# Kernel optimization log

Measured on AMD Instinct MI355X. Metric: run time of the kernel, lower is better.

Reference implementation:

```python
import jax, jax.numpy as jnp
import numpy as np

B, G, D, L, NH = 4, 30, 320, 4, 8
DK = D // NH
S = G * G
FF = 4 * D
EPS = 1e-5

FLOAT_KEYS = ['pe', 'in_emb_w', 'in_emb_b', 'wq', 'bq', 'wk', 'bk', 'wv', 'bv', 'wo', 'bo',
              'ln_a_g', 'ln_a_b', 'dist_emb', 'dir_emb', 'w_rot', 'b_rot', 'w_refl', 'b_refl',
              'w_tr', 'b_tr', 'w_sc', 'b_sc', 'tn_w1', 'tn_b1', 'tn_w2', 'tn_b2', 'tn_w3', 'tn_b3',
              'ff_w1', 'ff_b1', 'ff_w2', 'ff_b2', 'ln2_g', 'ln2_b', 'ck1', 'cb1', 'ck3', 'cb3',
              'ck5', 'cb5', 'ck7', 'cb7', 'fus_w', 'fus_b', 'op_w1', 'op_b1', 'op_w2', 'op_b2',
              'op_w3', 'op_b3']


def _make_pe():
    # Faithful vectorization of GeometricPositionalEncoding's triple loop.
    pe = np.zeros((G, G, D), dtype=np.float32)
    i = np.arange(0, D // 2, 2)                       # 0,2,...,158
    div = 10000.0 ** (i / D)
    h = np.arange(G, dtype=np.float64)
    sh = np.sin(h[:, None] / div)[:, None, :]
    ch = np.cos(h[:, None] / div)[:, None, :]
    pe[:, :, i] = sh
    pe[:, :, i + 1] = ch
    sw = np.sin(h[:, None] / div)[None, :, :]
    cw = np.cos(h[:, None] / div)[None, :, :]
    pe[:, :, i + D // 2] = sw
    pe[:, :, i + D // 2 + 1] = cw
    hh, ww = np.meshgrid(np.arange(G), np.arange(G), indexing='ij')
    c = G // 2
    pe[:, :, -4] = np.sqrt((hh - c) ** 2 + (ww - c) ** 2) / G   # overwrites last 4 dims, as in torch
    pe[:, :, -3] = hh / G
    pe[:, :, -2] = ww / G
    pe[:, :, -1] = (hh + ww) / (2 * G)
    return pe


def _make_geo_indices():
    # Precompute _compute_geometric_bias index tables (distance bin, direction octant).
    idx = np.arange(S)
    hc, wc = idx // G, idx % G
    dh = hc[None, :] - hc[:, None]                    # h2 - h1 at [i, j]
    dw = wc[None, :] - wc[:, None]
    dist = np.minimum(np.sqrt(dh ** 2 + dw ** 2).astype(np.int32), 59)
    ang = np.arctan2(dh.astype(np.float64), dw.astype(np.float64))
    dirn = ((ang + np.pi) / (2 * np.pi / 8)).astype(np.int32) % 8
    dirn[(dh == 0) & (dw == 0)] = 0
    return dist.astype(np.int32), dirn.astype(np.int32)


def _ln(x, g, b):
    m = x.mean(-1, keepdims=True)
    v = ((x - m) ** 2).mean(-1, keepdims=True)
    return (x - m) * jax.lax.rsqrt(v + EPS) * g + b


def _gelu(x):
    return jax.nn.gelu(x, approximate=False)  # torch nn.GELU default (erf)


def _forward(p, input_grid, dist_idx, dir_idx):
    x = jax.nn.one_hot(input_grid[:, 0], 10, dtype=jnp.float32)   # [B,G,G,10]
    x = x @ p['in_emb_w'] + p['in_emb_b']                          # [B,G,G,D]
    x = x + p['pe'][None]
    scale = 1.0 / np.sqrt(DK)
    for l in range(L):
        xs = x.reshape(B, S, D)
        def heads(w, b):
            return (xs @ w + b).reshape(B, S, NH, DK).transpose(0, 2, 1, 3)
        q = heads(p['wq'][l], p['bq'][l])
        k = heads(p['wk'][l], p['bk'][l])
        v = heads(p['wv'][l], p['bv'][l])
        # geometric bias via embedding gathers: [S,S,NH] -> [NH,S,S]
        bias = p['dist_emb'][l][dist_idx] + p['dir_emb'][l][dir_idx]
        scores = jnp.einsum('bhsd,bhtd->bhst', q, k) * scale + bias.transpose(2, 0, 1)[None]
        attn = jax.nn.softmax(scores, axis=-1)
        out = jnp.einsum('bhst,bhtd->bhsd', attn, v).transpose(0, 2, 1, 3).reshape(B, S, D)
        xs = _ln(out @ p['wo'][l] + p['bo'][l] + xs, p['ln_a_g'][l], p['ln_a_b'][l])
        # geometric transformation module
        g = xs.mean(1)                                              # [B,D] global mean over H,W
        tp = jnp.concatenate([
            jax.nn.softmax(g @ p['w_rot'][l] + p['b_rot'][l], axis=-1),
            jax.nn.softmax(g @ p['w_refl'][l] + p['b_refl'][l], axis=-1),
            jnp.tanh(g @ p['w_tr'][l] + p['b_tr'][l]),
            jax.nn.softmax(g @ p['w_sc'][l] + p['b_sc'][l], axis=-1)], axis=-1)   # [B,17]
        ti = jnp.concatenate([xs, jnp.broadcast_to(tp[:, None, :], (B, S, 17))], axis=-1)
        t = _gelu(ti @ p['tn_w1'][l] + p['tn_b1'][l])
        t = _gelu(t @ p['tn_w2'][l] + p['tn_b2'][l])
        t = t @ p['tn_w3'][l] + p['tn_b3'][l]
        xs = xs + 0.3 * t
        # feed-forward with post-LN residual
        f = _gelu(xs @ p['ff_w1'][l] + p['ff_b1'][l]) @ p['ff_w2'][l] + p['ff_b2'][l]
        xs = _ln(f + xs, p['ln2_g'][l], p['ln2_b'][l])
        x = xs.reshape(B, G, G, D)
    # multiscale conv fusion (NHWC, SAME padding == torch padding=k//2 for odd k)
    dn = ('NHWC', 'HWIO', 'NHWC')
    feats = [jax.nn.relu(jax.lax.conv_general_dilated(x, p['ck%d' % kk], (1, 1), 'SAME',
                                                      dimension_numbers=dn) + p['cb%d' % kk])
             for kk in (1, 3, 5, 7)]
    fused = jnp.concatenate(feats, axis=-1) @ p['fus_w'] + p['fus_b']
    h1 = _gelu(fused @ p['op_w1'] + p['op_b1'])
    h2 = _gelu(h1 @ p['op_w2'] + p['op_b2'])
    return h2 @ p['op_w3'] + p['op_b3']                            # [B,G,G,10] logits


def setup_inputs():
    key = jax.random.key(0)
    ks = iter(jax.random.split(key, 80))
    w = lambda *s: (0.02 * jax.random.normal(next(ks), s)).astype(jnp.float32)
    z = lambda *s: jnp.zeros(s, jnp.float32)
    inp = dict(
        input_grid=jax.random.randint(next(ks), (B, 1, G, G), 0, 10, dtype=jnp.int32),
        pe=jnp.asarray(_make_pe()),
        in_emb_w=w(10, D), in_emb_b=z(D),
        wq=w(L, D, D), bq=z(L, D), wk=w(L, D, D), bk=z(L, D),
        wv=w(L, D, D), bv=z(L, D), wo=w(L, D, D), bo=z(L, D),
        ln_a_g=jnp.ones((L, D), jnp.float32), ln_a_b=z(L, D),
        dist_emb=w(L, 60, NH), dir_emb=w(L, 8, NH),
        w_rot=w(L, D, 4), b_rot=z(L, 4), w_refl=w(L, D, 8), b_refl=z(L, 8),
        w_tr=w(L, D, 2), b_tr=z(L, 2), w_sc=w(L, D, 3), b_sc=z(L, 3),
        tn_w1=w(L, D + 17, 2 * D), tn_b1=z(L, 2 * D),
        tn_w2=w(L, 2 * D, D), tn_b2=z(L, D),
        tn_w3=w(L, D, D), tn_b3=z(L, D),
        ff_w1=w(L, D, FF), ff_b1=z(L, FF), ff_w2=w(L, FF, D), ff_b2=z(L, D),
        ln2_g=jnp.ones((L, D), jnp.float32), ln2_b=z(L, D),
        ck1=w(1, 1, D, D), cb1=z(D), ck3=w(3, 3, D, D), cb3=z(D),
        ck5=w(5, 5, D, D), cb5=z(D), ck7=w(7, 7, D, D), cb7=z(D),
        fus_w=w(4 * D, D), fus_b=z(D),
        op_w1=w(D, D // 2), op_b1=z(D // 2),
        op_w2=w(D // 2, D // 4), op_b2=z(D // 4),
        op_w3=w(D // 4, 10), op_b3=z(10),
    )
    di, dr = _make_geo_indices()
    inp['dist_idx'] = jnp.asarray(di)
    inp['dir_idx'] = jnp.asarray(dr)
    return inp


def reference(input_grid, dist_idx, dir_idx, pe, in_emb_w, in_emb_b, wq, bq, wk, bk, wv, bv, wo, bo,
              ln_a_g, ln_a_b, dist_emb, dir_emb, w_rot, b_rot, w_refl, b_refl, w_tr, b_tr, w_sc, b_sc,
              tn_w1, tn_b1, tn_w2, tn_b2, tn_w3, tn_b3, ff_w1, ff_b1, ff_w2, ff_b2, ln2_g, ln2_b,
              ck1, cb1, ck3, cb3, ck5, cb5, ck7, cb7, fus_w, fus_b,
              op_w1, op_b1, op_w2, op_b2, op_w3, op_b3):
    p = dict(zip(FLOAT_KEYS, (pe, in_emb_w, in_emb_b, wq, bq, wk, bk, wv, bv, wo, bo,
                              ln_a_g, ln_a_b, dist_emb, dir_emb, w_rot, b_rot, w_refl, b_refl,
                              w_tr, b_tr, w_sc, b_sc, tn_w1, tn_b1, tn_w2, tn_b2, tn_w3, tn_b3,
                              ff_w1, ff_b1, ff_w2, ff_b2, ln2_g, ln2_b, ck1, cb1, ck3, cb3,
                              ck5, cb5, ck7, cb7, fus_w, fus_b, op_w1, op_b1, op_w2, op_b2,
                              op_w3, op_b3)))
    return _forward(p, input_grid, dist_idx, dir_idx)
```

## Files before the change

### kernel.cpp

```cpp
#include <hip/hip_runtime.h>
#include <hip/hip_bf16.h>

#define BB 4
#define GG_ 30
#define DD 320
#define LL 4
#define NHH 8
#define DKK 40
#define SS 900
#define BS 3600
#define FFD 1280
#define LDK 72

typedef __attribute__((ext_vector_type(8))) short short8;
typedef __attribute__((ext_vector_type(4))) short short4v;
typedef __attribute__((ext_vector_type(4))) float f32x4;

__device__ __forceinline__ float gelu_f(float x) {
    return 0.5f * x * (1.0f + erff(x * 0.70710678118654752f));
}

__device__ __forceinline__ float bfbits2f(short b) {
    return __uint_as_float(((unsigned)(unsigned short)b) << 16);
}

__device__ __forceinline__ void convt_tile(const float* __restrict__ s,
                                           __hip_bfloat16* __restrict__ d,
                                           int K, int N, int Kpad, int kb, int nb) {
    __shared__ float t[32][33];
    const int tx = threadIdx.x, ty = threadIdx.y;
#pragma unroll
    for (int i = 0; i < 4; ++i) {
        int k = kb + ty + i * 8, n = nb + tx;
        t[ty + i * 8][tx] = (k < K && n < N) ? s[(size_t)k * N + n] : 0.f;
    }
    __syncthreads();
#pragma unroll
    for (int i = 0; i < 4; ++i) {
        int n = nb + ty + i * 8, k = kb + tx;
        if (n < N && k < Kpad) d[(size_t)n * Kpad + k] = __float2bfloat16(t[tx][ty + i * 8]);
    }
}

__global__ __launch_bounds__(256) void allconvt_kernel(
    const float* wo, const float* tnw1, const float* tnw2, const float* tnw3,
    const float* ffw1, const float* ffw2, const float* ck1, const float* ck3,
    const float* ck5, const float* ck7, const float* fusw, const float* opw1,
    __hip_bfloat16* WOT, __hip_bfloat16* TN1T, __hip_bfloat16* TN2T, __hip_bfloat16* TN3T,
    __hip_bfloat16* FF1T, __hip_bfloat16* FF2T, __hip_bfloat16* CK1T, __hip_bfloat16* CK3T,
    __hip_bfloat16* CK5T, __hip_bfloat16* CK7T, __hip_bfloat16* FUST, __hip_bfloat16* OP1T) {
    const int bid = blockIdx.x;
    const float* s; __hip_bfloat16* d;
    int K, N, Kpad, gx, per, local, sS, dS;
    if (bid < 400)        { local = bid;         s = wo;   d = WOT;  K = 320;  N = 320;  Kpad = 320;  sS = 102400; dS = 102400; gx = 10;  per = 100; }
    else if (bid < 1360)  { local = bid - 400;   s = tnw1; d = TN1T; K = 337;  N = 640;  Kpad = 384;  sS = 215680; dS = 245760; gx = 12;  per = 240; }
    else if (bid < 2160)  { local = bid - 1360;  s = tnw2; d = TN2T; K = 640;  N = 320;  Kpad = 640;  sS = 204800; dS = 204800; gx = 20;  per = 200; }
    else if (bid < 2560)  { local = bid - 2160;  s = tnw3; d = TN3T; K = 320;  N = 320;  Kpad = 320;  sS = 102400; dS = 102400; gx = 10;  per = 100; }
    else if (bid < 4160)  { local = bid - 2560;  s = ffw1; d = FF1T; K = 320;  N = 1280; Kpad = 320;  sS = 409600; dS = 409600; gx = 10;  per = 400; }
    else if (bid < 5760)  { local = bid - 4160;  s = ffw2; d = FF2T; K = 1280; N = 320;  Kpad = 1280; sS = 409600; dS = 409600; gx = 40;  per = 400; }
    else if (bid < 5860)  { local = bid - 5760;  s = ck1;  d = CK1T; K = 320;  N = 320;  Kpad = 320;  sS = 0; dS = 0; gx = 10;  per = 100; }
    else if (bid < 6760)  { local = bid - 5860;  s = ck3;  d = CK3T; K = 2880; N = 320;  Kpad = 2880; sS = 0; dS = 0; gx = 90;  per = 900; }
    else if (bid < 9260)  { local = bid - 6760;  s = ck5;  d = CK5T; K = 8000; N = 320;  Kpad = 8000; sS = 0; dS = 0; gx = 250; per = 2500; }
    else if (bid < 14160) { local = bid - 9260;  s = ck7;  d = CK7T; K = 15680; N = 320; Kpad = 15680; sS = 0; dS = 0; gx = 490; per = 4900; }
    else if (bid < 14560) { local = bid - 14160; s = fusw; d = FUST; K = 1280; N = 320;  Kpad = 1280; sS = 0; dS = 0; gx = 40;  per = 400; }
    else                  { local = bid - 14560; s = opw1; d = OP1T; K = 320;  N = 160;  Kpad = 320;  sS = 0; dS = 0; gx = 10;  per = 50; }
    const int mat = local / per, rem = local - mat * per;
    const int kb = (rem % gx) * 32, nb = (rem / gx) * 32;
    convt_tile(s + (size_t)mat * sS, d + (size_t)mat * dS, K, N, Kpad, kb, nb);
}

__global__ __launch_bounds__(256) void qkvconvt_kernel(const float* __restrict__ wq,
                                                       const float* __restrict__ wk,
                                                       const float* __restrict__ wv,
                                                       __hip_bfloat16* __restrict__ dst) {
    __shared__ float t[32][33];
    const int z = blockIdx.z, l = z / 3, wsel = z % 3;
    const float* s = (wsel == 0 ? wq : wsel == 1 ? wk : wv) + (size_t)l * 102400;
    __hip_bfloat16* d = dst + (size_t)l * 307200 + wsel * 102400;
    const int kb = blockIdx.x * 32, nb = blockIdx.y * 32;
    const int tx = threadIdx.x, ty = threadIdx.y;
#pragma unroll
    for (int i = 0; i < 4; ++i) {
        int k = kb + ty + i * 8, n = nb + tx;
        t[ty + i * 8][tx] = s[(size_t)k * 320 + n];
    }
    __syncthreads();
#pragma unroll
    for (int i = 0; i < 4; ++i) {
        int n = nb + ty + i * 8, k = kb + tx;
        d[(size_t)n * 320 + k] = __float2bfloat16(t[tx][ty + i * 8]);
    }
}

__global__ void embed_kernel(const int* __restrict__ grid, const float* __restrict__ pe,
                             const float* __restrict__ ew, const float* __restrict__ eb,
                             float* __restrict__ x, __hip_bfloat16* __restrict__ xb) {
    int idx = blockIdx.x * 256 + threadIdx.x;
    int m = idx / DD, d = idx % DD;
    int gv = grid[m];
    float v = ew[gv * DD + d] + eb[d] + pe[(m % SS) * DD + d];
    x[idx] = v;
    xb[idx] = __float2bfloat16(v);
}

__global__ __launch_bounds__(256) void mgemm_kernel(
    const __hip_bfloat16* __restrict__ A, int lda,
    const __hip_bfloat16* __restrict__ Wt, int ldw,
    const float* __restrict__ bias, const float* __restrict__ biasB, const float* __restrict__ biasC,
    const float* __restrict__ res, int ldr,
    float alpha, float* __restrict__ Cf, float* __restrict__ Cf2,
    __hip_bfloat16* __restrict__ Cb, int ldc,
    int M, int N, int K, int act) {
    __shared__ short As[128 * LDK];
    __shared__ short Bs[64 * LDK];
    const int tid = threadIdx.x;
    const int m0 = blockIdx.y * 128, n0 = blockIdx.x * 64;
    const int kb0 = blockIdx.z * K;
    float* __restrict__ CfO = (blockIdx.z == 0) ? Cf : Cf2;
    const int lane = tid & 63;
    const int w = tid >> 6, wm = w >> 1, wn = w & 1;
    const int rbase = tid >> 3, q8 = (tid & 7) * 8;
    f32x4 acc[4][2];
    const f32x4 fz = {0.f, 0.f, 0.f, 0.f};
#pragma unroll
    for (int mi = 0; mi < 4; ++mi)
#pragma unroll
        for (int ni = 0; ni < 2; ++ni) acc[mi][ni] = fz;
    const short8 zz = {0, 0, 0, 0, 0, 0, 0, 0};
    for (int k0 = 0; k0 < K; k0 += 64) {
#pragma unroll
        for (int c = 0; c < 4; ++c) {
            int r = c * 32 + rbase, m = m0 + r;
            short8 v = zz;
            if (m < M) v = *(const short8*)((const short*)A + (size_t)m * lda + kb0 + k0 + q8);
            *(short8*)(As + r * LDK + q8) = v;
        }
#pragma unroll
        for (int c = 0; c < 2; ++c) {
            int r = c * 32 + rbase, n = n0 + r;
            short8 v = zz;
            if (n < N) v = *(const short8*)((const short*)Wt + (size_t)n * ldw + kb0 + k0 + q8);
            *(short8*)(Bs + r * LDK + q8) = v;
        }
        __syncthreads();
#pragma unroll
        for (int ks = 0; ks < 64; ks += 32) {
            const int kb = ks + (lane >> 4) * 8;
            short8 af[4], bf[2];
#pragma unroll
            for (int mi = 0; mi < 4; ++mi)
                af[mi] = *(const short8*)(As + (wm * 64 + mi * 16 + (lane & 15)) * LDK + kb);
#pragma unroll
            for (int ni = 0; ni < 2; ++ni)
                bf[ni] = *(const short8*)(Bs + (wn * 32 + ni * 16 + (lane & 15)) * LDK + kb);
#pragma unroll
            for (int mi = 0; mi < 4; ++mi)
#pragma unroll
                for (int ni = 0; ni < 2; ++ni)
                    acc[mi][ni] = __builtin_amdgcn_mfma_f32_16x16x32_bf16(af[mi], bf[ni], acc[mi][ni], 0, 0, 0);
        }
        __syncthreads();
    }
    const int col0 = n0 + wn * 32 + (lane & 15);
    const int rloc = (lane >> 4) * 4;
#pragma unroll
    for (int mi = 0; mi < 4; ++mi) {
#pragma unroll
        for (int ni = 0; ni < 2; ++ni) {
            int col = col0 + ni * 16;
            if (col >= N) continue;
            float bv;
            if (biasC) bv = (col < 320) ? bias[col] : (col < 640) ? biasB[col - 320] : biasC[col - 640];
            else bv = bias ? bias[col] : 0.f;
#pragma unroll
            for (int r = 0; r < 4; ++r) {
                int row = m0 + wm * 64 + mi * 16 + rloc + r;
                if (row >= M) continue;
                float v = acc[mi][ni][r] + bv;
                if (act == 1) v = gelu_f(v);
                else if (act == 2) v = fmaxf(v, 0.f);
                v *= alpha;
                if (res) v += res[(size_t)row * ldr + col];
                if (CfO) CfO[(size_t)row * ldc + col] = v;
                if (Cb) Cb[(size_t)row * ldc + col] = __float2bfloat16(v);
            }
        }
    }
}

template <int KS>
__global__ __launch_bounds__(256) void mconv_kernel(
    const __hip_bfloat16* __restrict__ P, const __hip_bfloat16* __restrict__ Wt,
    __hip_bfloat16* __restrict__ part, int kh0step) {
    const int K = KS * KS * DD;
    const int OFF = 3 - KS / 2;
    const int kh0 = blockIdx.z * kh0step;
    const int nkh = (KS - kh0 < kh0step) ? (KS - kh0) : kh0step;
    const int Ksub = nkh * KS * DD;
    const int wbase = kh0 * KS * DD;
    __hip_bfloat16* __restrict__ Cp = part + (size_t)blockIdx.z * BS * DD;
    __shared__ short As[128 * LDK];
    __shared__ short Bs[64 * LDK];
    const int tid = threadIdx.x;
    const int m0 = blockIdx.y * 128, n0 = blockIdx.x * 64;
    const int lane = tid & 63;
    const int w = tid >> 6, wm = w >> 1, wn = w & 1;
    const int rbase = tid >> 3, q8 = (tid & 7) * 8;
    f32x4 acc[4][2];
    const f32x4 fz = {0.f, 0.f, 0.f, 0.f};
#pragma unroll
    for (int mi = 0; mi < 4; ++mi)
#pragma unroll
        for (int ni = 0; ni < 2; ++ni) acc[mi][ni] = fz;
    const short8 zz = {0, 0, 0, 0, 0, 0, 0, 0};
    for (int k0 = 0; k0 < Ksub; k0 += 64) {
#pragma unroll
        for (int c = 0; c < 4; ++c) {
            int r = c * 32 + rbase, m = m0 + r;
            int k = k0 + q8;
            int ci = k % DD, t = k / DD;
            int kw = t % KS, kh = kh0 + t / KS;
            short8 v = zz;
            if (m < BS) {
                int b = m / SS, hw = m % SS, oh = hw / GG_, ow = hw % GG_;
                int ih = oh + kh + OFF, iw = ow + kw + OFF;
                v = *(const short8*)((const short*)P + (((b * 36 + ih) * 36 + iw) * DD + ci));
            }
            *(short8*)(As + r * LDK + q8) = v;
        }
#pragma unroll
        for (int c = 0; c < 2; ++c) {
            int r = c * 32 + rbase, n = n0 + r;
            short8 v = *(const short8*)((const short*)Wt + (size_t)n * K + wbase + k0 + q8);
            *(short8*)(Bs + r * LDK + q8) = v;
        }
        __syncthreads();
#pragma unroll
        for (int ks = 0; ks < 64; ks += 32) {
            const int kb = ks + (lane >> 4) * 8;
            short8 af[4], bf[2];
#pragma unroll
            for (int mi = 0; mi < 4; ++mi)
                af[mi] = *(const short8*)(As + (wm * 64 + mi * 16 + (lane & 15)) * LDK + kb);
#pragma unroll
            for (int ni = 0; ni < 2; ++ni)
                bf[ni] = *(const short8*)(Bs + (wn * 32 + ni * 16 + (lane & 15)) * LDK + kb);
#pragma unroll
            for (int mi = 0; mi < 4; ++mi)
#pragma unroll
                for (int ni = 0; ni < 2; ++ni)
                    acc[mi][ni] = __builtin_amdgcn_mfma_f32_16x16x32_bf16(af[mi], bf[ni], acc[mi][ni], 0, 0, 0);
        }
        __syncthreads();
    }
    const int col0 = n0 + wn * 32 + (lane & 15);
    const int rloc = (lane >> 4) * 4;
#pragma unroll
    for (int mi = 0; mi < 4; ++mi) {
#pragma unroll
        for (int ni = 0; ni < 2; ++ni) {
            int col = col0 + ni * 16;
#pragma unroll
            for (int r = 0; r < 4; ++r) {
                int row = m0 + wm * 64 + mi * 16 + rloc + r;
                if (row < BS) Cp[(size_t)row * DD + col] = __float2bfloat16(acc[mi][ni][r]);
            }
        }
    }
}

__global__ __launch_bounds__(256) void creduce_kernel(const __hip_bfloat16* __restrict__ part,
                                                      int nsplit, const float* __restrict__ bias,
                                                      __hip_bfloat16* __restrict__ outb, int ldc) {
    int idx = blockIdx.x * 256 + threadIdx.x;
    if (idx >= BS * DD / 8) return;
    int row = idx / (DD / 8), c8 = (idx % (DD / 8)) * 8;
    float s[8] = {};
    for (int p = 0; p < nsplit; ++p) {
        short8 v = *(const short8*)((const short*)part + (size_t)p * BS * DD + (size_t)row * DD + c8);
#pragma unroll
        for (int j = 0; j < 8; ++j) s[j] += bfbits2f(v[j]);
    }
    __hip_bfloat16* o = outb + (size_t)row * ldc + c8;
#pragma unroll
    for (int j = 0; j < 8; ++j) o[j] = __float2bfloat16(fmaxf(s[j] + bias[c8 + j], 0.f));
}

__global__ void pad_kernel(const __hip_bfloat16* __restrict__ xb, __hip_bfloat16* __restrict__ p) {
    int idx = blockIdx.x * 256 + threadIdx.x;
    if (idx >= BB * 36 * 36 * DD) return;
    int c = idx % DD, t = idx / DD;
    int wp = t % 36, t2 = t / 36, hp = t2 % 36, b = t2 / 36;
    __hip_bfloat16 v = __float2bfloat16(0.f);
    if (hp >= 3 && hp < 33 && wp >= 3 && wp < 33)
        v = xb[((b * SS + (hp - 3) * GG_ + (wp - 3))) * DD + c];
    p[idx] = v;
}

__global__ __launch_bounds__(256) void gemm_kernel(
    const float* __restrict__ A, int lda, const float* __restrict__ W,
    const float* __restrict__ bias, float* __restrict__ C, int ldc,
    int M, int N, int K, int act) {
    __shared__ float As[16][65];
    __shared__ float Ws[16][65];
    const int tid = threadIdx.x;
    const int m0 = blockIdx.y * 64, n0 = blockIdx.x * 64;
    const int tx = tid & 15, ty = tid >> 4;
    float acc[4][4] = {};
    const int kkA = tid & 15, mloc0 = tid >> 4;
    const int nloc = tid & 63, kk0 = tid >> 6;
    for (int k0 = 0; k0 < K; k0 += 16) {
        const int kA = k0 + kkA;
#pragma unroll
        for (int i = 0; i < 4; ++i) {
            int mloc = mloc0 + i * 16, m = m0 + mloc;
            As[kkA][mloc] = (m < M && kA < K) ? A[m * lda + kA] : 0.f;
        }
#pragma unroll
        for (int i = 0; i < 4; ++i) {
            int kk = kk0 + i * 4, k = k0 + kk, n = n0 + nloc;
            Ws[kk][nloc] = (k < K && n < N) ? W[k * N + n] : 0.f;
        }
        __syncthreads();
#pragma unroll
        for (int kk = 0; kk < 16; ++kk) {
            float a[4], b[4];
#pragma unroll
            for (int i = 0; i < 4; ++i) a[i] = As[kk][ty * 4 + i];
#pragma unroll
            for (int j = 0; j < 4; ++j) b[j] = Ws[kk][tx * 4 + j];
#pragma unroll
            for (int i = 0; i < 4; ++i)
#pragma unroll
                for (int j = 0; j < 4; ++j) acc[i][j] = fmaf(a[i], b[j], acc[i][j]);
        }
        __syncthreads();
    }
#pragma unroll
    for (int i = 0; i < 4; ++i) {
        int m = m0 + ty * 4 + i;
        if (m >= M) continue;
#pragma unroll
        for (int j = 0; j < 4; ++j) {
            int n = n0 + tx * 4 + j;
            if (n >= N) continue;
            float v = acc[i][j] + bias[n];
            if (act == 1) v = gelu_f(v);
            C[m * ldc + n] = v;
        }
    }
}

__global__ __launch_bounds__(256) void attprep_kernel(const float* __restrict__ de,
                                                      const float* __restrict__ dre,
                                                      const int* __restrict__ dist,
                                                      const int* __restrict__ dirn,
                                                      const __hip_bfloat16* __restrict__ QKV,
                                                      __hip_bfloat16* __restrict__ biasOut,
                                                      __hip_bfloat16* __restrict__ VT) {
    const int gid = blockIdx.x;
    const int tid = threadIdx.x;
    if (gid < 27000) {
        const int h = gid / 3375;
        int idx = (gid % 3375) * 256 + tid;
        int sq = idx / 960, t = idx - sq * 960;
        float v = 0.f;
        if (t < SS) v = de[dist[sq * SS + t] * NHH + h] + dre[dirn[sq * SS + t] * NHH + h];
        biasOut[((size_t)h * SS + sq) * 960 + t] = __float2bfloat16(v);
    } else {
        int idx = (gid - 27000) * 256 + tid;
        int t = idx % 960;
        int d = (idx / 960) % 48;
        int h = (idx / (960 * 48)) % NHH;
        int b = idx / (960 * 48 * NHH);
        __hip_bfloat16 v = __float2bfloat16(0.f);
        if (t < SS && d < DKK) v = QKV[((size_t)b * SS + t) * 960 + 640 + h * DKK + d];
        VT[idx] = v;
    }
}

#define LQ 56
#define LK 56
#define LV 72
#define LP 72
__global__ __launch_bounds__(256) void mattn_kernel(
    const __hip_bfloat16* __restrict__ Qg, const __hip_bfloat16* __restrict__ Kg,
    const __hip_bfloat16* __restrict__ VTg, const __hip_bfloat16* __restrict__ BIASg,
    __hip_bfloat16* __restrict__ AO) {
    const int qt = blockIdx.x, h = blockIdx.y, b = blockIdx.z;
    const int tid = threadIdx.x, lane = tid & 63, w = tid >> 6;
    const int lhi = lane >> 4, llo = lane & 15;
    __shared__ short Qs[64 * LQ];
    __shared__ short Ks[64 * LK];
    __shared__ short Vs[48 * LV];
    __shared__ short Ps[4][16 * LP];
    short* Ps_w = Ps[w];
    const int q0 = qt * 64;
    const short4v z4 = {0, 0, 0, 0};
    const f32x4 fz = {0.f, 0.f, 0.f, 0.f};
    const float scale = 0.15811388300841898f;

    for (int task = tid; task < 64 * 14; task += 256) {
        int r = task / 14, d0 = (task - r * 14) * 4;
        int q = q0 + r;
        short4v v = z4;
        if (q < SS && d0 < DKK)
            v = *(const short4v*)((const short*)Qg + ((size_t)b * SS + q) * 960 + h * DKK + d0);
        *(short4v*)(Qs + r * LQ + d0) = v;
    }
    __syncthreads();
    short8 qa[2];
#pragma unroll
    for (int ks = 0; ks < 2; ++ks)
        qa[ks] = *(const short8*)(Qs + (w * 16 + llo) * LQ + ks * 32 + lhi * 8);

    float mrow[4] = {-1e30f, -1e30f, -1e30f, -1e30f};
    float lrow[4] = {0.f, 0.f, 0.f, 0.f};
    f32x4 o[3] = {fz, fz, fz};
    const int qrow = q0 + w * 16 + lhi * 4;

    for (int t = 0; t < 15; ++t) {
        const int kv0 = t * 64;
        for (int task = tid; task < 64 * 14; task += 256) {
            int r = task / 14, d0 = (task - r * 14) * 4;
            int kv = kv0 + r;
            short4v v = z4;
            if (kv < SS && d0 < DKK)
                v = *(const short4v*)((const short*)Kg + ((size_t)b * SS + kv) * 960 + h * DKK + d0);
            *(short4v*)(Ks + r * LK + d0) = v;
        }
        for (int task = tid; task < 48 * 16; task += 256) {
            int r = task / 16, c4 = (task - r * 16) * 4;
            short4v v = *(const short4v*)((const short*)VTg +
                         (((size_t)b * NHH + h) * 48 + r) * 960 + kv0 + c4);
            *(short4v*)(Vs + r * LV + c4) = v;
        }
        __syncthreads();
        f32x4 s[4] = {fz, fz, fz, fz};
#pragma unroll
        for (int ks = 0; ks < 2; ++ks) {
#pragma unroll
            for (int ni = 0; ni < 4; ++ni) {
                short8 kb = *(const short8*)(Ks + (ni * 16 + llo) * LK + ks * 32 + lhi * 8);
                s[ni] = __builtin_amdgcn_mfma_f32_16x16x32_bf16(qa[ks], kb, s[ni], 0, 0, 0);
            }
        }
#pragma unroll
        for (int ni = 0; ni < 4; ++ni) {
            int col = kv0 + ni * 16 + llo;
#pragma unroll
            for (int r = 0; r < 4; ++r) {
                int qc = qrow + r; if (qc > SS - 1) qc = SS - 1;
                float v = s[ni][r] * scale +
                          __bfloat162float(BIASg[((size_t)h * SS + qc) * 960 + col]);
                s[ni][r] = (col < SS) ? v : -1e30f;
            }
        }
        float rmax[4], psum[4], corr[4];
#pragma unroll
        for (int r = 0; r < 4; ++r)
            rmax[r] = fmaxf(fmaxf(s[0][r], s[1][r]), fmaxf(s[2][r], s[3][r]));
#pragma unroll
        for (int off = 1; off < 16; off <<= 1)
#pragma unroll
            for (int r = 0; r < 4; ++r)
                rmax[r] = fmaxf(rmax[r], __shfl_xor(rmax[r], off));
#pragma unroll
        for (int r = 0; r < 4; ++r) {
            float mnew = fmaxf(mrow[r], rmax[r]);
            corr[r] = expf(mrow[r] - mnew);
            mrow[r] = mnew;
            float ps = 0.f;
#pragma unroll
            for (int ni = 0; ni < 4; ++ni) {
                float p = expf(s[ni][r] - mnew);
                s[ni][r] = p;
                ps += p;
            }
            psum[r] = ps;
        }
#pragma unroll
        for (int off = 1; off < 16; off <<= 1)
#pragma unroll
            for (int r = 0; r < 4; ++r) psum[r] += __shfl_xor(psum[r], off);
#pragma unroll
        for (int r = 0; r < 4; ++r) lrow[r] = lrow[r] * corr[r] + psum[r];
#pragma unroll
        for (int nj = 0; nj < 3; ++nj)
#pragma unroll
            for (int r = 0; r < 4; ++r) o[nj][r] *= corr[r];
#pragma unroll
        for (int ni = 0; ni < 4; ++ni)
#pragma unroll
            for (int r = 0; r < 4; ++r)
                ((__hip_bfloat16*)Ps_w)[(lhi * 4 + r) * LP + ni * 16 + llo] =
                    __float2bfloat16(s[ni][r]);
#pragma unroll
        for (int ks = 0; ks < 2; ++ks) {
            short8 pa = *(const short8*)(Ps_w + llo * LP + ks * 32 + lhi * 8);
#pragma unroll
            for (int nj = 0; nj < 3; ++nj) {
                short8 vb = *(const short8*)(Vs + (nj * 16 + llo) * LV + ks * 32 + lhi * 8);
                o[nj] = __builtin_amdgcn_mfma_f32_16x16x32_bf16(pa, vb, o[nj], 0, 0, 0);
            }
        }
        __syncthreads();
    }
#pragma unroll
    for (int nj = 0; nj < 3; ++nj) {
        int d = nj * 16 + llo;
        if (d >= DKK) continue;
#pragma unroll
        for (int r = 0; r < 4; ++r) {
            int q = qrow + r;
            if (q < SS)
                AO[((size_t)b * SS + q) * DD + h * DKK + d] = __float2bfloat16(o[nj][r] / lrow[r]);
        }
    }
}

__global__ __launch_bounds__(320) void ln_kernel(const float* __restrict__ a,
                                                 const float* __restrict__ a2,
                                                 const float* __restrict__ cb,
                                                 const float* __restrict__ add,
                                                 const float* __restrict__ g,
                                                 const float* __restrict__ bta,
                                                 float* __restrict__ out,
                                                 __hip_bfloat16* __restrict__ outb) {
    const int row = blockIdx.x, i = threadIdx.x;
    __shared__ float red[320];
    __shared__ float s_m, s_v;
    float v = a[row * DD + i];
    if (a2) v += a2[row * DD + i];
    if (cb) v += cb[i];
    if (add) v += add[row * DD + i];
    red[i] = v;
    __syncthreads();
    if (i < 64) red[i] += red[i + 256];
    __syncthreads();
    for (int s = 128; s > 0; s >>= 1) {
        if (i < s) red[i] += red[i + s];
        __syncthreads();
    }
    if (i == 0) s_m = red[0] * (1.0f / DD);
    __syncthreads();
    const float d = v - s_m;
    red[i] = d * d;
    __syncthreads();
    if (i < 64) red[i] += red[i + 256];
    __syncthreads();
    for (int s = 128; s > 0; s >>= 1) {
        if (i < s) red[i] += red[i + s];
        __syncthreads();
    }
    if (i == 0) s_v = red[0] * (1.0f / DD);
    __syncthreads();
    float o = d * rsqrtf(s_v + 1e-5f) * g[i] + bta[i];
    out[row * DD + i] = o;
    outb[row * DD + i] = __float2bfloat16(o);
}

__global__ __launch_bounds__(256) void mpart_kernel(const float* __restrict__ xs,
                                                    float* __restrict__ mp) {
    const int b = blockIdx.y, z = blockIdx.z;
    const int d = blockIdx.x * 64 + (threadIdx.x & 63);
    const int rg = threadIdx.x >> 6;
    float s = 0.f;
    const int t0 = z * 150;
    for (int t = t0 + rg; t < t0 + 150; t += 4) s += xs[((size_t)b * SS + t) * DD + d];
    __shared__ float red[256];
    red[threadIdx.x] = s;
    __syncthreads();
    if (threadIdx.x < 128) red[threadIdx.x] += red[threadIdx.x + 128];
    __syncthreads();
    if (threadIdx.x < 64) mp[((size_t)b * 6 + z) * DD + d] = red[threadIdx.x] + red[threadIdx.x + 64];
}

__global__ __launch_bounds__(64) void tp_kernel(const float* __restrict__ mp,
                                                const float* __restrict__ wrot, const float* __restrict__ brot,
                                                const float* __restrict__ wrefl, const float* __restrict__ brefl,
                                                const float* __restrict__ wtr, const float* __restrict__ btr,
                                                const float* __restrict__ wsc, const float* __restrict__ bsc,
                                                float* __restrict__ tp) {
    const int b = blockIdx.x, tid = threadIdx.x;
    __shared__ float gs[DD];
    __shared__ float raw[17];
    for (int j = tid; j < DD; j += 64) {
        float s6 = 0.f;
#pragma unroll
        for (int z = 0; z < 6; ++z) s6 += mp[((size_t)b * 6 + z) * DD + j];
        gs[j] = s6 * (1.0f / SS);
    }
    __syncthreads();
    if (tid < 17) {
        float s;
        if (tid < 4) {
            s = brot[tid];
            for (int d = 0; d < DD; ++d) s = fmaf(gs[d], wrot[d * 4 + tid], s);
        } else if (tid < 12) {
            int j = tid - 4;
            s = brefl[j];
            for (int d = 0; d < DD; ++d) s = fmaf(gs[d], wrefl[d * 8 + j], s);
        } else if (tid < 14) {
            int j = tid - 12;
            s = btr[j];
            for (int d = 0; d < DD; ++d) s = fmaf(gs[d], wtr[d * 2 + j], s);
        } else {
            int j = tid - 14;
            s = bsc[j];
            for (int d = 0; d < DD; ++d) s = fmaf(gs[d], wsc[d * 3 + j], s);
        }
        raw[tid] = s;
    }
    __syncthreads();
    if (tid == 0) {
        float mx = -1e30f;
        for (int j = 0; j < 4; ++j) mx = fmaxf(mx, raw[j]);
        float sm = 0.f, e[4];
        for (int j = 0; j < 4; ++j) { e[j] = expf(raw[j] - mx); sm += e[j]; }
        for (int j = 0; j < 4; ++j) tp[b * 17 + j] = e[j] / sm;
    } else if (tid == 1) {
        float mx = -1e30f;
        for (int j = 4; j < 12; ++j) mx = fmaxf(mx, raw[j]);
        float sm = 0.f, e[8];
        for (int j = 0; j < 8; ++j) { e[j] = expf(raw[4 + j] - mx); sm += e[j]; }
        for (int j = 0; j < 8; ++j) tp[b * 17 + 4 + j] = e[j] / sm;
    } else if (tid == 2) {
        tp[b * 17 + 12] = tanhf(raw[12]);
        tp[b * 17 + 13] = tanhf(raw[13]);
    } else if (tid == 3) {
        float mx = -1e30f;
        for (int j = 14; j < 17; ++j) mx = fmaxf(mx, raw[j]);
        float sm = 0.f, e[3];
        for (int j = 0; j < 3; ++j) { e[j] = expf(raw[14 + j] - mx); sm += e[j]; }
        for (int j = 0; j < 3; ++j) tp[b * 17 + 14 + j] = e[j] / sm;
    }
}

__global__ void concat_kernel(const __hip_bfloat16* __restrict__ xb, const float* __restrict__ tp,
                              __hip_bfloat16* __restrict__ ti) {
    int idx = blockIdx.x * 256 + threadIdx.x;
    if (idx >= BS * 384) return;
    int m = idx / 384, j = idx % 384;
    __hip_bfloat16 v;
    if (j < DD) v = xb[m * DD + j];
    else if (j < 337) v = __float2bfloat16(tp[(m / SS) * 17 + (j - DD)]);
    else v = __float2bfloat16(0.f);
    ti[idx] = v;
}

static inline void launch_mgemm(hipStream_t s, const __hip_bfloat16* A, int lda,
                                const __hip_bfloat16* Wt, int ldw, const float* bias,
                                const float* biasB, const float* biasC,
                                const float* res, int ldr, float alpha, float* Cf,
                                __hip_bfloat16* Cb, int ldc, int M, int N, int K, int act) {
    dim3 g((N + 63) / 64, (M + 127) / 128);
    mgemm_kernel<<<g, 256, 0, s>>>(A, lda, Wt, ldw, bias, biasB, biasC, res, ldr, alpha,
                                   Cf, nullptr, Cb, ldc, M, N, K, act);
}

extern "C" void kernel_launch(void* const* d_in, const int* in_sizes, int n_in,
                              void* d_out, int out_size, void* d_ws, size_t ws_size,
                              hipStream_t stream) {
    (void)in_sizes; (void)n_in; (void)out_size; (void)ws_size;
    const int* in_grid = (const int*)d_in[0];
    const float* pe = (const float*)d_in[1];
    const float* iew = (const float*)d_in[2];
    const float* ieb = (const float*)d_in[3];
    const float* wq = (const float*)d_in[4], *bq = (const float*)d_in[5];
    const float* wk = (const float*)d_in[6], *bk = (const float*)d_in[7];
    const float* wv = (const float*)d_in[8], *bv = (const float*)d_in[9];
    const float* wo = (const float*)d_in[10], *bo = (const float*)d_in[11];
    const float* lnag = (const float*)d_in[12], *lnab = (const float*)d_in[13];
    const float* dist_emb = (const float*)d_in[14], *dir_emb = (const float*)d_in[15];
    const float* wrot = (const float*)d_in[16], *brot = (const float*)d_in[17];
    const float* wrefl = (const float*)d_in[18], *brefl = (const float*)d_in[19];
    const float* wtr = (const float*)d_in[20], *btr = (const float*)d_in[21];
    const float* wsc = (const float*)d_in[22], *bsc = (const float*)d_in[23];
    const float* tnw1 = (const float*)d_in[24], *tnb1 = (const float*)d_in[25];
    const float* tnw2 = (const float*)d_in[26], *tnb2 = (const float*)d_in[27];
    const float* tnw3 = (const float*)d_in[28], *tnb3 = (const float*)d_in[29];
    const float* ffw1 = (const float*)d_in[30], *ffb1 = (const float*)d_in[31];
    const float* ffw2 = (const float*)d_in[32], *ffb2 = (const float*)d_in[33];
    const float* ln2g = (const float*)d_in[34], *ln2b = (const float*)d_in[35];
    const float* ck1 = (const float*)d_in[36], *cb1 = (const float*)d_in[37];
    const float* ck3 = (const float*)d_in[38], *cb3 = (const float*)d_in[39];
    const float* ck5 = (const float*)d_in[40], *cb5 = (const float*)d_in[41];
    const float* ck7 = (const float*)d_in[42], *cb7 = (const float*)d_in[43];
    const float* fusw = (const float*)d_in[44], *fusb = (const float*)d_in[45];
    const float* opw1 = (const float*)d_in[46], *opb1 = (const float*)d_in[47];
    const float* opw2 = (const float*)d_in[48], *opb2 = (const float*)d_in[49];
    const float* opw3 = (const float*)d_in[50], *opb3 = (const float*)d_in[51];
    const int* dist_idx = (const int*)d_in[52];
    const int* dir_idx = (const int*)d_in[53];
    float* out = (float*)d_out;

    char* base = (char*)d_ws;
    typedef __hip_bfloat16 bf;
    bf* WQKVT = (bf*)(base + 0);
    bf* WOT = (bf*)(base + 2457600);
    bf* TN1T = (bf*)(base + 3276800);
    bf* TN2T = (bf*)(base + 5242880);
    bf* TN3T = (bf*)(base + 6881280);
    bf* FF1T = (bf*)(base + 7700480);
    bf* FF2T = (bf*)(base + 10977280);
    bf* CK1T = (bf*)(base + 14254080);
    bf* CK3T = (bf*)(base + 14458880);
    bf* CK5T = (bf*)(base + 16302080);
    bf* CK7T = (bf*)(base + 21422080);
    bf* FUST = (bf*)(base + 31457280);
    bf* OP1T = (bf*)(base + 32276480);
    float* XS = (float*)(base + 32378880);
    bf* XSbf = (bf*)(base + 36986880);
    bf* QKVbf = (bf*)(base + 39290880);
    bf* VT = (bf*)(base + 46202880);
    float* P1f = (float*)(base + 39290880);
    float* R2 = (float*)(base + 53114880);
    float* TP = (float*)(base + 57728000);
    bf* CPART = (bf*)(base + 39290880);
    char* BIG = base + 57728512;
    bf* AObf = (bf*)(BIG + 0);
    float* MPart = (float*)(BIG + 0);
    bf* BIAS = (bf*)(BIG + 2764800);
    bf* TIbf = (bf*)(BIG + 0);
    bf* T1bf = (bf*)(BIG + 2764800);
    bf* T2bf = (bf*)(BIG + 7372800);
    bf* F1bf = (bf*)(BIG + 0);
    bf* PADbf = (bf*)(BIG + 0);
    bf* FEATSbf = (bf*)(BIG + 3317760);
    float* H1 = (float*)(BIG + 0);
    float* H2 = (float*)(BIG + 2304000);
    bf* R2bf = XSbf;

    dim3 cb(32, 8);
    qkvconvt_kernel<<<dim3(10, 10, 12), cb, 0, stream>>>(wq, wk, wv, WQKVT);
    allconvt_kernel<<<14610, cb, 0, stream>>>(wo, tnw1, tnw2, tnw3, ffw1, ffw2,
                                              ck1, ck3, ck5, ck7, fusw, opw1,
                                              WOT, TN1T, TN2T, TN3T, FF1T, FF2T,
                                              CK1T, CK3T, CK5T, CK7T, FUST, OP1T);

    embed_kernel<<<4500, 256, 0, stream>>>(in_grid, pe, iew, ieb, XS, XSbf);

    for (int l = 0; l < LL; ++l) {
        const int wO = l * DD * DD, bO = l * DD;
        launch_mgemm(stream, XSbf, DD, WQKVT + l * 307200, 320, bq + bO, bk + bO, bv + bO,
                     nullptr, 0, 1.f, nullptr, QKVbf, 960, BS, 960, 320, 0);
        attprep_kernel<<<32760, 256, 0, stream>>>(dist_emb + l * 60 * NHH, dir_emb + l * 8 * NHH,
                                                  dist_idx, dir_idx, QKVbf, BIAS, VT);
        mattn_kernel<<<dim3(15, NHH, BB), 256, 0, stream>>>(QKVbf, QKVbf + 320, VT, BIAS, AObf);
        launch_mgemm(stream, AObf, DD, WOT + wO, DD, bo + bO, nullptr, nullptr, XS, DD, 1.f,
                     R2, nullptr, DD, BS, DD, DD, 0);
        ln_kernel<<<BS, 320, 0, stream>>>(R2, nullptr, nullptr, nullptr, lnag + bO, lnab + bO, XS, XSbf);
        mpart_kernel<<<dim3(5, BB, 6), 256, 0, stream>>>(XS, MPart);
        tp_kernel<<<BB, 64, 0, stream>>>(MPart, wrot + l * 1280, brot + l * 4,
                                         wrefl + l * 2560, brefl + l * 8,
                                         wtr + l * 640, btr + l * 2,
                                         wsc + l * 960, bsc + l * 3, TP);
        concat_kernel<<<(BS * 384 + 255) / 256, 256, 0, stream>>>(XSbf, TP, TIbf);
        launch_mgemm(stream, TIbf, 384, TN1T + l * 245760, 384, tnb1 + l * 640, nullptr, nullptr,
                     nullptr, 0, 1.f, nullptr, T1bf, 640, BS, 640, 384, 1);
        launch_mgemm(stream, T1bf, 640, TN2T + l * 204800, 640, tnb2 + bO, nullptr, nullptr,
                     nullptr, 0, 1.f, nullptr, T2bf, DD, BS, DD, 640, 1);
        launch_mgemm(stream, T2bf, DD, TN3T + wO, DD, tnb3 + bO, nullptr, nullptr, XS, DD, 0.3f,
                     XS, XSbf, DD, BS, DD, DD, 0);
        launch_mgemm(stream, XSbf, DD, FF1T + l * 409600, DD, ffb1 + l * FFD, nullptr, nullptr,
                     nullptr, 0, 1.f, nullptr, F1bf, FFD, BS, FFD, DD, 1);
        {
            dim3 g(5, 29, 2);
            mgemm_kernel<<<g, 256, 0, stream>>>(F1bf, FFD, FF2T + l * 409600, FFD,
                                                nullptr, nullptr, nullptr, nullptr, 0, 1.f,
                                                R2, P1f, nullptr, DD, BS, DD, 640, 0);
        }
        ln_kernel<<<BS, 320, 0, stream>>>(R2, P1f, ffb2 + bO, XS, ln2g + bO, ln2b + bO, XS, XSbf);
    }

    pad_kernel<<<(BB * 36 * 36 * DD + 255) / 256, 256, 0, stream>>>(XSbf, PADbf);
    launch_mgemm(stream, XSbf, DD, CK1T, DD, cb1, nullptr, nullptr, nullptr, 0, 1.f,
                 nullptr, FEATSbf + 0, 1280, BS, DD, DD, 2);
    const int RED = (BS * DD / 8 + 255) / 256;
    mconv_kernel<3><<<dim3(5, 29, 3), 256, 0, stream>>>(PADbf, CK3T, CPART, 1);
    creduce_kernel<<<RED, 256, 0, stream>>>(CPART, 3, cb3, FEATSbf + 320, 1280);
    mconv_kernel<5><<<dim3(5, 29, 5), 256, 0, stream>>>(PADbf, CK5T, CPART, 1);
    creduce_kernel<<<RED, 256, 0, stream>>>(CPART, 5, cb5, FEATSbf + 640, 1280);
    mconv_kernel<7><<<dim3(5, 29, 7), 256, 0, stream>>>(PADbf, CK7T, CPART, 1);
    creduce_kernel<<<RED, 256, 0, stream>>>(CPART, 7, cb7, FEATSbf + 960, 1280);
    launch_mgemm(stream, FEATSbf, 1280, FUST, 1280, fusb, nullptr, nullptr, nullptr, 0, 1.f,
                 nullptr, R2bf, DD, BS, DD, 1280, 0);
    launch_mgemm(stream, R2bf, DD, OP1T, DD, opb1, nullptr, nullptr, nullptr, 0, 1.f,
                 H1, nullptr, 160, BS, 160, DD, 1);
    gemm_kernel<<<dim3(2, 57), 256, 0, stream>>>(H1, 160, opw2, opb2, H2, 80, BS, 80, 160, 1);
    gemm_kernel<<<dim3(1, 57), 256, 0, stream>>>(H2, 80, opw3, opb3, out, 10, BS, 10, 80, 0);
}
```

Baseline: 1.743 ms.

## Split attention KV loop across two wave groups and swap conv grid order

The attention kernel now runs 512 threads per block. Two groups of four waves each handle alternate 64-key tiles, and their partial softmax states (max, sum, output) are merged through shared memory at the end. This is meant to double the parallelism per query tile, since the grid is only 480 blocks. It also switches to fast __expf and widens the Q/K LDS stride to 72. Separately, the mconv kernel swaps its grid x/y mapping so M tiles vary fastest, which changes L2 reuse of weights versus activations. The attention kernel uses more LDS and adds extra syncs in exchange.

```diff
diff --git a/kernel.cpp b/kernel.cpp
--- a/kernel.cpp
+++ b/kernel.cpp
@@ -202,7 +202,7 @@
     __shared__ short As[128 * LDK];
     __shared__ short Bs[64 * LDK];
     const int tid = threadIdx.x;
-    const int m0 = blockIdx.y * 128, n0 = blockIdx.x * 64;
+    const int m0 = blockIdx.x * 128, n0 = blockIdx.y * 64;
     const int lane = tid & 63;
     const int w = tid >> 6, wm = w >> 1, wn = w & 1;
     const int rbase = tid >> 3, q8 = (tid & 7) * 8;
@@ -379,29 +379,36 @@
     }
 }
 
-#define LQ 56
-#define LK 56
+#define LQ 72
+#define LK 72
 #define LV 72
 #define LP 72
-__global__ __launch_bounds__(256) void mattn_kernel(
+__global__ __launch_bounds__(512) void mattn_kernel(
     const __hip_bfloat16* __restrict__ Qg, const __hip_bfloat16* __restrict__ Kg,
     const __hip_bfloat16* __restrict__ VTg, const __hip_bfloat16* __restrict__ BIASg,
     __hip_bfloat16* __restrict__ AO) {
     const int qt = blockIdx.x, h = blockIdx.y, b = blockIdx.z;
     const int tid = threadIdx.x, lane = tid & 63, w = tid >> 6;
+    const int wq = w & 3, ws = w >> 2;
+    const int tid2 = tid & 255;
     const int lhi = lane >> 4, llo = lane & 15;
     __shared__ short Qs[64 * LQ];
-    __shared__ short Ks[64 * LK];
-    __shared__ short Vs[48 * LV];
-    __shared__ short Ps[4][16 * LP];
+    __shared__ short Ks[2][64 * LK];
+    __shared__ short Vs[2][48 * LV];
+    __shared__ short Ps[8][16 * LP];
+    __shared__ float Lm[4][16];
+    __shared__ float Ll[4][16];
+    __shared__ float Lo[4][16][DKK];
     short* Ps_w = Ps[w];
+    short* Ks_s = Ks[ws];
+    short* Vs_s = Vs[ws];
     const int q0 = qt * 64;
     const short4v z4 = {0, 0, 0, 0};
     const f32x4 fz = {0.f, 0.f, 0.f, 0.f};
     const float scale = 0.15811388300841898f;
 
-    for (int task = tid; task < 64 * 14; task += 256) {
-        int r = task / 14, d0 = (task - r * 14) * 4;
+    for (int task = tid; task < 64 * 16; task += 512) {
+        int r = task >> 4, d0 = (task & 15) * 4;
         int q = q0 + r;
         short4v v = z4;
         if (q < SS && d0 < DKK)
@@ -412,109 +419,136 @@
     short8 qa[2];
 #pragma unroll
     for (int ks = 0; ks < 2; ++ks)
-        qa[ks] = *(const short8*)(Qs + (w * 16 + llo) * LQ + ks * 32 + lhi * 8);
+        qa[ks] = *(const short8*)(Qs + (wq * 16 + llo) * LQ + ks * 32 + lhi * 8);
 
     float mrow[4] = {-1e30f, -1e30f, -1e30f, -1e30f};
     float lrow[4] = {0.f, 0.f, 0.f, 0.f};
     f32x4 o[3] = {fz, fz, fz};
-    const int qrow = q0 + w * 16 + lhi * 4;
-
-    for (int t = 0; t < 15; ++t) {
+    const int qrow = q0 + wq * 16 + lhi * 4;
+
+    for (int tt = 0; tt < 8; ++tt) {
+        const int t = tt * 2 + ws;
         const int kv0 = t * 64;
-        for (int task = tid; task < 64 * 14; task += 256) {
-            int r = task / 14, d0 = (task - r * 14) * 4;
-            int kv = kv0 + r;
-            short4v v = z4;
-            if (kv < SS && d0 < DKK)
-                v = *(const short4v*)((const short*)Kg + ((size_t)b * SS + kv) * 960 + h * DKK + d0);
-            *(short4v*)(Ks + r * LK + d0) = v;
-        }
-        for (int task = tid; task < 48 * 16; task += 256) {
-            int r = task / 16, c4 = (task - r * 16) * 4;
-            short4v v = *(const short4v*)((const short*)VTg +
-                         (((size_t)b * NHH + h) * 48 + r) * 960 + kv0 + c4);
-            *(short4v*)(Vs + r * LV + c4) = v;
-        }
-        __syncthreads();
-        f32x4 s[4] = {fz, fz, fz, fz};
-#pragma unroll
-        for (int ks = 0; ks < 2; ++ks) {
+        if (t < 15) {
+            for (int task = tid2; task < 64 * 16; task += 256) {
+                int r = task >> 4, d0 = (task & 15) * 4;
+                int kv = kv0 + r;
+                short4v v = z4;
+                if (kv < SS && d0 < DKK)
+                    v = *(const short4v*)((const short*)Kg + ((size_t)b * SS + kv) * 960 + h * DKK + d0);
+                *(short4v*)(Ks_s + r * LK + d0) = v;
+            }
+            for (int task = tid2; task < 48 * 16; task += 256) {
+                int r = task >> 4, c4 = (task & 15) * 4;
+                short4v v = *(const short4v*)((const short*)VTg +
+                             (((size_t)b * NHH + h) * 48 + r) * 960 + kv0 + c4);
+                *(short4v*)(Vs_s + r * LV + c4) = v;
+            }
+        }
+        __syncthreads();
+        if (t < 15) {
+            f32x4 s[4] = {fz, fz, fz, fz};
+#pragma unroll
+            for (int ks = 0; ks < 2; ++ks) {
+#pragma unroll
+                for (int ni = 0; ni < 4; ++ni) {
+                    short8 kb = *(const short8*)(Ks_s + (ni * 16 + llo) * LK + ks * 32 + lhi * 8);
+                    s[ni] = __builtin_amdgcn_mfma_f32_16x16x32_bf16(qa[ks], kb, s[ni], 0, 0, 0);
+                }
+            }
 #pragma unroll
             for (int ni = 0; ni < 4; ++ni) {
-                short8 kb = *(const short8*)(Ks + (ni * 16 + llo) * LK + ks * 32 + lhi * 8);
-                s[ni] = __builtin_amdgcn_mfma_f32_16x16x32_bf16(qa[ks], kb, s[ni], 0, 0, 0);
-            }
-        }
-#pragma unroll
-        for (int ni = 0; ni < 4; ++ni) {
-            int col = kv0 + ni * 16 + llo;
+                int col = kv0 + ni * 16 + llo;
+#pragma unroll
+                for (int r = 0; r < 4; ++r) {
+                    int qc = qrow + r; if (qc > SS - 1) qc = SS - 1;
+                    float v = s[ni][r] * scale +
+                              __bfloat162float(BIASg[((size_t)h * SS + qc) * 960 + col]);
+                    s[ni][r] = (col < SS) ? v : -1e30f;
+                }
+            }
+            float rmax[4], psum[4], corr[4];
+#pragma unroll
+            for (int r = 0; r < 4; ++r)
+                rmax[r] = fmaxf(fmaxf(s[0][r], s[1][r]), fmaxf(s[2][r], s[3][r]));
+#pragma unroll
+            for (int off = 1; off < 16; off <<= 1)
+#pragma unroll
+                for (int r = 0; r < 4; ++r)
+                    rmax[r] = fmaxf(rmax[r], __shfl_xor(rmax[r], off));
 #pragma unroll
             for (int r = 0; r < 4; ++r) {
-                int qc = qrow + r; if (qc > SS - 1) qc = SS - 1;
-                float v = s[ni][r] * scale +
-                          __bfloat162float(BIASg[((size_t)h * SS + qc) * 960 + col]);
-                s[ni][r] = (col < SS) ? v : -1e30f;
-            }
-        }
-        float rmax[4], psum[4], corr[4];
-#pragma unroll
-        for (int r = 0; r < 4; ++r)
-            rmax[r] = fmaxf(fmaxf(s[0][r], s[1][r]), fmaxf(s[2][r], s[3][r]));
-#pragma unroll
-        for (int off = 1; off < 16; off <<= 1)
-#pragma unroll
-            for (int r = 0; r < 4; ++r)
-                rmax[r] = fmaxf(rmax[r], __shfl_xor(rmax[r], off));
+                float mnew = fmaxf(mrow[r], rmax[r]);
+                corr[r] = __expf(mrow[r] - mnew);
+                mrow[r] = mnew;
+                float ps = 0.f;
+#pragma unroll
+                for (int ni = 0; ni < 4; ++ni) {
+                    float p = __expf(s[ni][r] - mnew);
+                    s[ni][r] = p;
+                    ps += p;
+                }
+                psum[r] = ps;
+            }
+#pragma unroll
+            for (int off = 1; off < 16; off <<= 1)
+#pragma unroll
+                for (int r = 0; r < 4; ++r) psum[r] += __shfl_xor(psum[r], off);
+#pragma unroll
+            for (int r = 0; r < 4; ++r) lrow[r] = lrow[r] * corr[r] + psum[r];
+#pragma unroll
+            for (int nj = 0; nj < 3; ++nj)
+#pragma unroll
+                for (int r = 0; r < 4; ++r) o[nj][r] *= corr[r];
+#pragma unroll
+            for (int ni = 0; ni < 4; ++ni)
+#pragma unroll
+                for (int r = 0; r < 4; ++r)
+                    ((__hip_bfloat16*)Ps_w)[(lhi * 4 + r) * LP + ni * 16 + llo] =
+                        __float2bfloat16(s[ni][r]);
+#pragma unroll
+            for (int ks = 0; ks < 2; ++ks) {
+                short8 pa = *(const short8*)(Ps_w + llo * LP + ks * 32 + lhi * 8);
+#pragma unroll
+                for (int nj = 0; nj < 3; ++nj) {
+                    short8 vb = *(const short8*)(Vs_s + (nj * 16 + llo) * LV + ks * 32 + lhi * 8);
+                    o[nj] = __builtin_amdgcn_mfma_f32_16x16x32_bf16(pa, vb, o[nj], 0, 0, 0);
+                }
+            }
+        }
+        __syncthreads();
+    }
+    if (ws == 1) {
 #pragma unroll
         for (int r = 0; r < 4; ++r) {
-            float mnew = fmaxf(mrow[r], rmax[r]);
-            corr[r] = expf(mrow[r] - mnew);
-            mrow[r] = mnew;
-            float ps = 0.f;
-#pragma unroll
-            for (int ni = 0; ni < 4; ++ni) {
-                float p = expf(s[ni][r] - mnew);
-                s[ni][r] = p;
-                ps += p;
-            }
-            psum[r] = ps;
-        }
-#pragma unroll
-        for (int off = 1; off < 16; off <<= 1)
-#pragma unroll
-            for (int r = 0; r < 4; ++r) psum[r] += __shfl_xor(psum[r], off);
-#pragma unroll
-        for (int r = 0; r < 4; ++r) lrow[r] = lrow[r] * corr[r] + psum[r];
-#pragma unroll
-        for (int nj = 0; nj < 3; ++nj)
-#pragma unroll
-            for (int r = 0; r < 4; ++r) o[nj][r] *= corr[r];
-#pragma unroll
-        for (int ni = 0; ni < 4; ++ni)
-#pragma unroll
-            for (int r = 0; r < 4; ++r)
-                ((__hip_bfloat16*)Ps_w)[(lhi * 4 + r) * LP + ni * 16 + llo] =
-                    __float2bfloat16(s[ni][r]);
-#pragma unroll
-        for (int ks = 0; ks < 2; ++ks) {
-            short8 pa = *(const short8*)(Ps_w + llo * LP + ks * 32 + lhi * 8);
+            int lr = lhi * 4 + r;
+            if (llo == 0) { Lm[wq][lr] = mrow[r]; Ll[wq][lr] = lrow[r]; }
 #pragma unroll
             for (int nj = 0; nj < 3; ++nj) {
-                short8 vb = *(const short8*)(Vs + (nj * 16 + llo) * LV + ks * 32 + lhi * 8);
-                o[nj] = __builtin_amdgcn_mfma_f32_16x16x32_bf16(pa, vb, o[nj], 0, 0, 0);
-            }
-        }
-        __syncthreads();
-    }
-#pragma unroll
-    for (int nj = 0; nj < 3; ++nj) {
-        int d = nj * 16 + llo;
-        if (d >= DKK) continue;
+                int d = nj * 16 + llo;
+                if (d < DKK) Lo[wq][lr][d] = o[nj][r];
+            }
+        }
+    }
+    __syncthreads();
+    if (ws == 0) {
 #pragma unroll
         for (int r = 0; r < 4; ++r) {
+            int lr = lhi * 4 + r;
+            float m1 = Lm[wq][lr], l1 = Ll[wq][lr];
+            float m = fmaxf(mrow[r], m1);
+            float a0 = __expf(mrow[r] - m), a1 = __expf(m1 - m);
+            float linv = 1.f / (lrow[r] * a0 + l1 * a1);
             int q = qrow + r;
-            if (q < SS)
-                AO[((size_t)b * SS + q) * DD + h * DKK + d] = __float2bfloat16(o[nj][r] / lrow[r]);
+            if (q < SS) {
+#pragma unroll
+                for (int nj = 0; nj < 3; ++nj) {
+                    int d = nj * 16 + llo;
+                    if (d < DKK)
+                        AO[((size_t)b * SS + q) * DD + h * DKK + d] =
+                            __float2bfloat16((o[nj][r] * a0 + Lo[wq][lr][d] * a1) * linv);
+                }
+            }
         }
     }
 }
@@ -747,7 +781,7 @@
                      nullptr, 0, 1.f, nullptr, QKVbf, 960, BS, 960, 320, 0);
         attprep_kernel<<<32760, 256, 0, stream>>>(dist_emb + l * 60 * NHH, dir_emb + l * 8 * NHH,
                                                   dist_idx, dir_idx, QKVbf, BIAS, VT);
-        mattn_kernel<<<dim3(15, NHH, BB), 256, 0, stream>>>(QKVbf, QKVbf + 320, VT, BIAS, AObf);
+        mattn_kernel<<<dim3(15, NHH, BB), 512, 0, stream>>>(QKVbf, QKVbf + 320, VT, BIAS, AObf);
         launch_mgemm(stream, AObf, DD, WOT + wO, DD, bo + bO, nullptr, nullptr, XS, DD, 1.f,
                      R2, nullptr, DD, BS, DD, DD, 0);
         ln_kernel<<<BS, 320, 0, stream>>>(R2, nullptr, nullptr, nullptr, lnag + bO, lnab + bO, XS, XSbf);
@@ -778,11 +812,11 @@
     launch_mgemm(stream, XSbf, DD, CK1T, DD, cb1, nullptr, nullptr, nullptr, 0, 1.f,
                  nullptr, FEATSbf + 0, 1280, BS, DD, DD, 2);
     const int RED = (BS * DD / 8 + 255) / 256;
-    mconv_kernel<3><<<dim3(5, 29, 3), 256, 0, stream>>>(PADbf, CK3T, CPART, 1);
+    mconv_kernel<3><<<dim3(29, 5, 3), 256, 0, stream>>>(PADbf, CK3T, CPART, 1);
     creduce_kernel<<<RED, 256, 0, stream>>>(CPART, 3, cb3, FEATSbf + 320, 1280);
-    mconv_kernel<5><<<dim3(5, 29, 5), 256, 0, stream>>>(PADbf, CK5T, CPART, 1);
+    mconv_kernel<5><<<dim3(29, 5, 5), 256, 0, stream>>>(PADbf, CK5T, CPART, 1);
     creduce_kernel<<<RED, 256, 0, stream>>>(CPART, 5, cb5, FEATSbf + 640, 1280);
-    mconv_kernel<7><<<dim3(5, 29, 7), 256, 0, stream>>>(PADbf, CK7T, CPART, 1);
+    mconv_kernel<7><<<dim3(29, 5, 7), 256, 0, stream>>>(PADbf, CK7T, CPART, 1);
     creduce_kernel<<<RED, 256, 0, stream>>>(CPART, 7, cb7, FEATSbf + 960, 1280);
     launch_mgemm(stream, FEATSbf, 1280, FUST, 1280, fusb, nullptr, nullptr, nullptr, 0, 1.f,
                  nullptr, R2bf, DD, BS, DD, 1280, 0);
```

New measurement: 1.610 ms. 1.08x faster.
